# Kernel optimization log

Hardware: AMD Instinct MI355X
Metric: run time of the kernel (lower is better)

## Reference

```python
import math
import jax, jax.numpy as jnp
import numpy as np

B, N, NR, DA, E, H, NB = 2, 2048, 256, 256, 768, 12, 2
DH = E // H
NQ, NK = 32, 128
INF = 1e10


def _layernorm(x, g=None, b=None, eps=1e-5):
    mu = x.mean(-1, keepdims=True)
    var = ((x - mu) ** 2).mean(-1, keepdims=True)
    y = (x - mu) * jax.lax.rsqrt(var + eps)
    if g is not None:
        y = y * g + b
    return y


def _fourier(x):
    # NeRF-style: freqs = 2**linspace(0,12,64); out dim = 3*(1+2*64) = 387
    freqs = 2.0 ** jnp.linspace(0.0, 12.0, 64)
    ang = (x[..., None, :] * freqs[:, None]).reshape(*x.shape[:-1], -1)  # (...,192)
    return jnp.concatenate([x, jnp.sin(ang), jnp.cos(ang)], -1)


def _abs_pos(pos):
    # sinusoidal absolute PE, embed_dim=DA//2, include_input -> DA//2 + 1 dims
    d = DA // 2
    div = jnp.exp(jnp.arange(0, d, 2, dtype=jnp.float32) * (-math.log(10000.0) / d))
    ang = pos * div  # (B,N,1)*(d/2,) -> (B,N,d/2)
    return jnp.concatenate([pos, jnp.sin(ang), jnp.cos(ang)], -1)


def _local_bias(n, nq, nk):
    # vectorized create_local_attn_bias: block-diagonal local window mask
    i = jnp.arange(n)
    blk = i // nq
    lo = jnp.maximum(0, nq * blk - (nk - nq) // 2)
    hi = nq * blk + (nq + nk) // 2
    j = jnp.arange(n)
    allowed = (j[None, :] >= lo[:, None]) & (j[None, :] < hi[:, None])
    return jnp.where(allowed, 0.0, -INF).astype(jnp.float32)


def _rope(x, pos):
    # x: (B,H,N,DH), pos: (B,N) float
    half = DH // 2
    inv = 1.0 / (10000.0 ** (jnp.arange(half, dtype=jnp.float32) / half))
    ang = pos[:, None, :, None] * inv  # (B,1,N,half)
    c, s = jnp.cos(ang), jnp.sin(ang)
    x1, x2 = x[..., :half], x[..., half:]
    return jnp.concatenate([x1 * c - x2 * s, x1 * s + x2 * c], -1)


def setup_inputs() -> dict:
    key = jax.random.key(0)
    def rn(i, shape, s=1.0):
        return jax.random.normal(jax.random.fold_in(key, i), shape, jnp.float32) * s
    LF = 387 + (DA // 2 + 1) + 408  # 924
    tok = (jnp.arange(N) * NR) // N  # each atom's residue index (sorted)
    inp = {
        'atom_coords': rn(0, (B, N, 3), 10.0),
        'ref_pos': rn(1, (B, N, 3), 10.0),
        'res_id': jnp.broadcast_to(tok[None, :, None], (B, N, 1)).astype(jnp.int32),
        'res_type_feat': rn(2, (B, N, 23)),
        'charge': rn(3, (B, N, 1)),
        'atomic_number': rn(4, (B, N, 128)),
        'atom_name_feat': rn(5, (B, N, 256)),
        'adaLN_emb': rn(6, (B, DA)),
        'rope_pos': jnp.broadcast_to(jnp.arange(N, dtype=jnp.int32)[None], (B, N)),
        'atom_to_token': jnp.broadcast_to(jax.nn.one_hot(tok, NR, dtype=jnp.float32)[None], (B, N, NR)),
        'feat_W': rn(7, (LF, DA), 0.02), 'feat_b': jnp.zeros(DA), 'feat_ln_g': jnp.ones(DA), 'feat_ln_b': jnp.zeros(DA),
        'pos_W': rn(8, (387, DA), 0.02),
        'in_W': rn(9, (2 * DA, DA), 0.02),
        'tin_W': rn(10, (DA, E), 0.02), 'tin_b': jnp.zeros(E), 'tin_ln_g': jnp.ones(E), 'tin_ln_b': jnp.zeros(E),
        'ada_W': rn(11, (DA, E), 0.02), 'ada_b': jnp.zeros(E), 'ada_ln_g': jnp.ones(E), 'ada_ln_b': jnp.zeros(E),
        'blk_mod_W': rn(12, (NB, E, 6 * E), 0.02), 'blk_mod_b': jnp.zeros((NB, 6 * E)),
        'blk_qkv_W': rn(13, (NB, E, 3 * E), 0.02), 'blk_qkv_b': jnp.zeros((NB, 3 * E)),
        'blk_o_W': rn(14, (NB, E, E), 0.02), 'blk_o_b': jnp.zeros((NB, E)),
        'blk_m1_W': rn(15, (NB, E, 4 * E), 0.02), 'blk_m1_b': jnp.zeros((NB, 4 * E)),
        'blk_m2_W': rn(16, (NB, 4 * E, E), 0.02), 'blk_m2_b': jnp.zeros((NB, E)),
        'tout_W': rn(17, (E, DA), 0.02), 'tout_b': jnp.zeros(DA), 'tout_ln_g': jnp.ones(DA), 'tout_ln_b': jnp.zeros(DA),
    }
    return inp


def reference(atom_coords, ref_pos, res_id, res_type_feat, charge, atomic_number,
              atom_name_feat, adaLN_emb, rope_pos, atom_to_token,
              feat_W, feat_b, feat_ln_g, feat_ln_b, pos_W, in_W,
              tin_W, tin_b, tin_ln_g, tin_ln_b, ada_W, ada_b, ada_ln_g, ada_ln_b,
              blk_mod_W, blk_mod_b, blk_qkv_W, blk_qkv_b, blk_o_W, blk_o_b,
              blk_m1_W, blk_m1_b, blk_m2_W, blk_m2_b,
              tout_W, tout_b, tout_ln_g, tout_ln_b):
    # feature fusion
    ref_pos_emb = _fourier(ref_pos)                                   # (B,N,387)
    atom_res_pos = _abs_pos(res_id.astype(jnp.float32))               # (B,N,129)
    feats = jnp.concatenate([ref_pos_emb, res_type_feat, atom_res_pos,
                             charge, atomic_number, atom_name_feat], -1)  # (B,N,924)
    feats = jax.nn.silu(_layernorm(feats @ feat_W + feat_b, feat_ln_g, feat_ln_b))
    coords = _fourier(atom_coords) @ pos_W                            # (B,N,DA)
    atom_in = jnp.concatenate([feats, coords], -1) @ in_W             # (B,N,DA)
    x = _layernorm(atom_in @ tin_W + tin_b, tin_ln_g, tin_ln_b)       # (B,N,E)
    c = _layernorm(adaLN_emb @ ada_W + ada_b, ada_ln_g, ada_ln_b)     # (B,E)

    bias = _local_bias(N, NQ, NK)                                     # (N,N)
    pos = rope_pos.astype(jnp.float32)
    scale = 1.0 / math.sqrt(DH)
    for l in range(NB):  # small fixed layer count
        m = jax.nn.silu(c) @ blk_mod_W[l] + blk_mod_b[l]
        sh1, sc1, g1, sh2, sc2, g2 = jnp.split(m, 6, -1)              # each (B,E)
        h = _layernorm(x) * (1 + sc1[:, None]) + sh1[:, None]
        qkv = (h @ blk_qkv_W[l] + blk_qkv_b[l]).reshape(B, N, 3, H, DH)
        q, k, v = [qkv[:, :, i].transpose(0, 2, 1, 3) for i in range(3)]  # (B,H,N,DH)
        q, k = _rope(q, pos), _rope(k, pos)
        scores = jnp.einsum('bhqd,bhkd->bhqk', q, k) * scale + bias
        attn = jax.nn.softmax(scores, -1)
        o = jnp.einsum('bhqk,bhkd->bhqd', attn, v).transpose(0, 2, 1, 3).reshape(B, N, E)
        x = x + g1[:, None] * (o @ blk_o_W[l] + blk_o_b[l])
        h2 = _layernorm(x) * (1 + sc2[:, None]) + sh2[:, None]
        x = x + g2[:, None] * (jax.nn.gelu(h2 @ blk_m1_W[l] + blk_m1_b[l]) @ blk_m2_W[l] + blk_m2_b[l])

    atom_latent = _layernorm(x @ tout_W + tout_b, tout_ln_g, tout_ln_b)   # (B,N,DA)
    a2t = atom_to_token / (atom_to_token.sum(1, keepdims=True) + 1e-6)    # segment-mean weights
    residue_latent = jnp.einsum('bnr,bnd->brd', a2t, atom_latent)         # (B,NR,DA)
    return residue_latent, atom_latent
```

## Files before the change

kernel.cpp:

```cpp
#include <hip/hip_runtime.h>
#include <hip/hip_bf16.h>
#include <math.h>

#define B_ 2
#define N_ 2048
#define NR_ 256
#define DA_ 256
#define E_ 768
#define H_ 12
#define DH_ 64
#define NB_ 2

typedef __attribute__((ext_vector_type(8))) __bf16 bf16x8;
typedef __attribute__((ext_vector_type(4))) float f32x4;

union U8 { bf16x8 v; __hip_bfloat16 e[8]; unsigned short u[8]; };
union U4 { __hip_bfloat16 e[4]; uint2 u2; };

__device__ __forceinline__ void gload16(const void* g, void* l) {
    __builtin_amdgcn_global_load_lds(
        (const __attribute__((address_space(1))) void*)g,
        (__attribute__((address_space(3))) void*)l, 16, 0, 0);
}

__global__ __launch_bounds__(128) void build_feats_kernel(
    const float* __restrict__ atom_coords, const float* __restrict__ ref_pos,
    const int* __restrict__ res_id, const float* __restrict__ res_type,
    const float* __restrict__ charge, const float* __restrict__ atomic_number,
    const float* __restrict__ atom_name, const int* __restrict__ rope_pos,
    __hip_bfloat16* __restrict__ feats, __hip_bfloat16* __restrict__ coordsF,
    float* __restrict__ ropeC, float* __restrict__ ropeS)
{
    int a = blockIdx.x;
    int tid = threadIdx.x;
    __hip_bfloat16* f  = feats   + (size_t)a * 1024;
    __hip_bfloat16* cf = coordsF + (size_t)a * 512;

    float rp[3], cc[3];
    #pragma unroll
    for (int i = 0; i < 3; ++i) { rp[i] = ref_pos[(size_t)a*3 + i]; cc[i] = atom_coords[(size_t)a*3 + i]; }

    if (tid < 3) { f[tid] = __float2bfloat16(rp[tid]); cf[tid] = __float2bfloat16(cc[tid]); }

    if (tid >= 64 && tid < 96) {
        int dd = tid - 64;
        float rpos = (float)rope_pos[a];
        float ang = rpos * expf(-0.28782313662425574f * (float)dd);
        float sn, cs; sincosf(ang, &sn, &cs);
        ropeC[a*32 + dd] = cs; ropeS[a*32 + dd] = sn;
    }

    for (int s = tid; s < 192; s += 128) {
        int fi = s / 3, ci = s % 3;
        float freq = exp2f(12.f * (float)fi / 63.f);
        float ar = rp[ci] * freq;
        float ac = cc[ci] * freq;
        float snr, csr, snc, csc_;
        sincosf(ar, &snr, &csr);
        sincosf(ac, &snc, &csc_);
        f[3 + s]    = __float2bfloat16(snr);  f[195 + s]  = __float2bfloat16(csr);
        cf[3 + s]   = __float2bfloat16(snc);  cf[195 + s] = __float2bfloat16(csc_);
    }
    if (tid < 23) f[387 + tid] = __float2bfloat16(res_type[(size_t)a*23 + tid]);

    float pos = (float)res_id[a];
    if (tid == 0) f[410] = __float2bfloat16(pos);
    if (tid < 64) {
        float div = expf(-9.210340371976184f / 128.f * (float)(2 * tid));
        float ang = pos * div;
        float sn, cs; sincosf(ang, &sn, &cs);
        f[411 + tid] = __float2bfloat16(sn);
        f[475 + tid] = __float2bfloat16(cs);
    }
    if (tid == 0) f[539] = __float2bfloat16(charge[a]);
    if (tid < 128) f[540 + tid] = __float2bfloat16(atomic_number[(size_t)a*128 + tid]);
    for (int s = tid; s < 256; s += 128) f[668 + s] = __float2bfloat16(atom_name[(size_t)a*256 + s]);
    if (tid < 100) f[924 + tid] = __float2bfloat16(0.f);
    if (tid < 125) cf[387 + tid] = __float2bfloat16(0.f);
}

__global__ __launch_bounds__(256) void transconv_kernel(
    const float* __restrict__ W, __hip_bfloat16* __restrict__ WT,
    int Ksrc, int Kdst, int Nn, size_t wstride, size_t tstride)
{
    __shared__ float t[32][33];
    W  += (size_t)blockIdx.z * wstride;
    WT += (size_t)blockIdx.z * tstride;
    int n0 = blockIdx.x * 32, k0 = blockIdx.y * 32;
    int tid = threadIdx.x;
    int tx = tid & 31, ty = tid >> 5;
    #pragma unroll
    for (int i = 0; i < 4; ++i) {
        int k = k0 + ty + i*8;
        t[ty + i*8][tx] = (k < Ksrc) ? W[(size_t)k * Nn + n0 + tx] : 0.f;
    }
    __syncthreads();
    #pragma unroll
    for (int i = 0; i < 4; ++i) {
        int row = ty + i*8;
        WT[(size_t)(n0 + row) * Kdst + k0 + tx] = __float2bfloat16(t[tx][row]);
    }
}

__device__ __forceinline__ float epi_apply(float v, int grow, int gcol,
    const float* bias, int mode, const float* X, int ldx,
    const float* gate, int gstride)
{
    if (bias) v += bias[gcol];
    if (mode == 1) {
        float u = 1.5957691216057308f * (v + 0.044715f * v * v * v);
        v = v / (1.f + __expf(-u));
    } else if (mode == 2) {
        int b = grow >> 11;
        v = X[(size_t)grow * ldx + gcol] + gate[(size_t)b * gstride + gcol] * v;
    } else if (mode == 3) {
        v = v * gate[grow];
    }
    return v;
}

__global__ __launch_bounds__(256) void gemm_bf16_kernel(
    const __hip_bfloat16* __restrict__ A, int lda,
    const __hip_bfloat16* __restrict__ BT, int ldb,
    const float* __restrict__ bias,
    void* __restrict__ C, int ldc,
    int K, int mode, int obf,
    const float* __restrict__ X, int ldx,
    const float* __restrict__ gate, int gstride,
    float* __restrict__ P,
    int mtiles, size_t bstrideA, size_t bstrideB)
{
    __shared__ __hip_bfloat16 As[3][128 * 32];
    __shared__ __hip_bfloat16 Bs[3][128 * 32];

    int gx = gridDim.x;
    int nwg = gx * gridDim.y;
    int fo = blockIdx.y * gx + blockIdx.x;
    int ft = (fo & 7) * (nwg >> 3) + (fo >> 3);
    int bx = ft % gx, by = ft / gx;

    int bb  = by / mtiles;
    int m0l = (by % mtiles) * 128;
    int m0g = by * 128;
    int n0 = bx * 128;
    const __hip_bfloat16* Ab  = A  + (size_t)bb * bstrideA;
    const __hip_bfloat16* BTb = BT + (size_t)bb * bstrideB;
    int nz = gridDim.z;
    int Kh = K / nz;
    int kb = blockIdx.z * Kh;
    int nIter = Kh >> 5;
    int tid = threadIdx.x;
    int w = tid >> 6, l = tid & 63;
    int wr = (w >> 1) * 64, wc = (w & 1) * 64;
    int lr = l & 15, lg = l >> 4;
    int slot = ((lg ^ ((lr >> 1) & 3)) & 3) * 8;

    int seg0 = tid,        row0s = seg0 >> 2, g0 = (seg0 & 3) ^ ((row0s >> 1) & 3);
    int seg1 = 256 + tid,  row1s = seg1 >> 2, g1 = (seg1 & 3) ^ ((row1s >> 1) & 3);

    f32x4 acc[4][4];
    #pragma unroll
    for (int i = 0; i < 4; ++i)
        #pragma unroll
        for (int j = 0; j < 4; ++j)
            acc[i][j] = f32x4{0.f, 0.f, 0.f, 0.f};

    {
        gload16(Ab  + (size_t)(m0l + row0s) * lda + kb + g0 * 8, (char*)As[0] + seg0 * 16);
        gload16(BTb + (size_t)(n0 + row0s) * ldb + kb + g0 * 8, (char*)Bs[0] + seg0 * 16);
        gload16(Ab  + (size_t)(m0l + row1s) * lda + kb + g1 * 8, (char*)As[0] + seg1 * 16);
        gload16(BTb + (size_t)(n0 + row1s) * ldb + kb + g1 * 8, (char*)Bs[0] + seg1 * 16);
        if (nIter > 1) {
            int k1 = kb + 32;
            gload16(Ab  + (size_t)(m0l + row0s) * lda + k1 + g0 * 8, (char*)As[1] + seg0 * 16);
            gload16(BTb + (size_t)(n0 + row0s) * ldb + k1 + g0 * 8, (char*)Bs[1] + seg0 * 16);
            gload16(Ab  + (size_t)(m0l + row1s) * lda + k1 + g1 * 8, (char*)As[1] + seg1 * 16);
            gload16(BTb + (size_t)(n0 + row1s) * ldb + k1 + g1 * 8, (char*)Bs[1] + seg1 * 16);
        }
    }

    int cur = 0;
    for (int it = 0; it < nIter; ++it) {
        if (it + 1 < nIter) asm volatile("s_waitcnt vmcnt(4)" ::: "memory");
        else                asm volatile("s_waitcnt vmcnt(0)" ::: "memory");
        __builtin_amdgcn_s_barrier();
        __builtin_amdgcn_sched_barrier(0);
        if (it + 2 < nIter) {
            int nb = cur + 2; if (nb >= 3) nb -= 3;
            int kn = kb + (it + 2) * 32;
            gload16(Ab  + (size_t)(m0l + row0s) * lda + kn + g0 * 8, (char*)As[nb] + seg0 * 16);
            gload16(BTb + (size_t)(n0 + row0s) * ldb + kn + g0 * 8, (char*)Bs[nb] + seg0 * 16);
            gload16(Ab  + (size_t)(m0l + row1s) * lda + kn + g1 * 8, (char*)As[nb] + seg1 * 16);
            gload16(BTb + (size_t)(n0 + row1s) * ldb + kn + g1 * 8, (char*)Bs[nb] + seg1 * 16);
        }
        bf16x8 af[4], bfr[4];
        #pragma unroll
        for (int i = 0; i < 4; ++i) {
            af[i]  = *(bf16x8*)(As[cur] + (wr + i*16 + lr) * 32 + slot);
            bfr[i] = *(bf16x8*)(Bs[cur] + (wc + i*16 + lr) * 32 + slot);
        }
        #pragma unroll
        for (int i = 0; i < 4; ++i)
            #pragma unroll
            for (int j = 0; j < 4; ++j)
                acc[i][j] = __builtin_amdgcn_mfma_f32_16x16x32_bf16(af[i], bfr[j], acc[i][j], 0, 0, 0);
        cur = (cur == 2) ? 0 : cur + 1;
    }

    if (nz > 1) {
        int Nw = gridDim.x * 128;
        size_t pstride = (size_t)Nw * (gridDim.y * 128);
        float* Pz = P + (size_t)blockIdx.z * pstride;
        #pragma unroll
        for (int i = 0; i < 4; ++i)
            #pragma unroll
            for (int j = 0; j < 4; ++j)
                #pragma unroll
                for (int r = 0; r < 4; ++r) {
                    int grow = m0g + wr + i*16 + lg*4 + r;
                    int gcol = n0 + wc + j*16 + lr;
                    Pz[(size_t)grow * Nw + gcol] = acc[i][j][r];
                }
        return;
    }

    #pragma unroll
    for (int i = 0; i < 4; ++i)
        #pragma unroll
        for (int j = 0; j < 4; ++j)
            #pragma unroll
            for (int r = 0; r < 4; ++r) {
                int grow = m0g + wr + i*16 + lg*4 + r;
                int gcol = n0 + wc + j*16 + lr;
                float v = epi_apply(acc[i][j][r], grow, gcol, bias, mode, X, ldx, gate, gstride);
                if (obf)
                    ((__hip_bfloat16*)C)[(size_t)grow * ldc + gcol] = __float2bfloat16(v);
                else
                    ((float*)C)[(size_t)grow * ldc + gcol] = v;
            }
}

__global__ __launch_bounds__(256) void gcomb_kernel(
    const float* __restrict__ P, size_t pstride, int nz, int Nw,
    const float* __restrict__ bias,
    void* __restrict__ C, int ldc, int mode, int obf,
    const float* __restrict__ X, int ldx,
    const float* __restrict__ gate, int gstride,
    __hip_bfloat16* __restrict__ C2, int ldc2)
{
    int idx = blockIdx.x * 256 + threadIdx.x;
    int e0 = idx * 4;
    int grow = e0 / Nw, gc0 = e0 % Nw;
    float4 v = *(const float4*)(P + (size_t)grow * Nw + gc0);
    for (int z = 1; z < nz; ++z) {
        float4 t = *(const float4*)(P + (size_t)z * pstride + (size_t)grow * Nw + gc0);
        v.x += t.x; v.y += t.y; v.z += t.z; v.w += t.w;
    }
    float e[4] = {v.x, v.y, v.z, v.w};
    #pragma unroll
    for (int r = 0; r < 4; ++r)
        e[r] = epi_apply(e[r], grow, gc0 + r, bias, mode, X, ldx, gate, gstride);
    if (obf) {
        U4 o4;
        #pragma unroll
        for (int r = 0; r < 4; ++r) o4.e[r] = __float2bfloat16(e[r]);
        *(uint2*)((__hip_bfloat16*)C + (size_t)grow * ldc + gc0) = o4.u2;
    } else {
        *(float4*)((float*)C + (size_t)grow * ldc + gc0) = make_float4(e[0], e[1], e[2], e[3]);
    }
    if (C2) {
        U4 o4;
        #pragma unroll
        for (int r = 0; r < 4; ++r) o4.e[r] = __float2bfloat16(e[r]);
        *(uint2*)(C2 + (size_t)grow * ldc2 + gc0) = o4.u2;
    }
}

__global__ __launch_bounds__(256) void combln256_kernel(
    const float* __restrict__ P, size_t pstride, int nz,
    const float* __restrict__ bias,
    const float* __restrict__ g, const float* __restrict__ bv,
    int do_silu, int obf,
    void* __restrict__ out, int ldout)
{
    int row = blockIdx.x, d = threadIdx.x;
    __shared__ float red[256];
    float v = P[(size_t)row*256 + d];
    for (int z = 1; z < nz; ++z) v += P[(size_t)z*pstride + (size_t)row*256 + d];
    v += bias[d];
    red[d] = v; __syncthreads();
    for (int off = 128; off > 0; off >>= 1) { if (d < off) red[d] += red[d+off]; __syncthreads(); }
    float mu = red[0] * (1.f/256.f);
    __syncthreads();
    float dv = v - mu;
    red[d] = dv*dv; __syncthreads();
    for (int off = 128; off > 0; off >>= 1) { if (d < off) red[d] += red[d+off]; __syncthreads(); }
    float rstd = rsqrtf(red[0] * (1.f/256.f) + 1e-5f);
    float y = dv * rstd * g[d] + bv[d];
    if (do_silu) y = y / (1.f + __expf(-y));
    if (obf) ((__hip_bfloat16*)out)[(size_t)row * ldout + d] = __float2bfloat16(y);
    else     ((float*)out)[(size_t)row * ldout + d] = y;
}

__global__ __launch_bounds__(256) void gcombln_kernel(
    const float* __restrict__ P, size_t pstride, int nz,
    const float* __restrict__ bias,
    float* __restrict__ X,
    const float* __restrict__ gate,
    const float* __restrict__ scm, const float* __restrict__ shm,
    __hip_bfloat16* __restrict__ Hb)
{
    int row = blockIdx.x, tid = threadIdx.x;
    int b = row >> 11;
    __shared__ float red[256];
    float xv[3];
    float s = 0.f;
    #pragma unroll
    for (int q = 0; q < 3; ++q) {
        int d = tid + q*256;
        float v = P[(size_t)row*768 + d];
        for (int z = 1; z < nz; ++z) v += P[(size_t)z*pstride + (size_t)row*768 + d];
        v += bias[d];
        v = X[(size_t)row*768 + d] + gate[(size_t)b*4608 + d] * v;
        X[(size_t)row*768 + d] = v;
        xv[q] = v; s += v;
    }
    red[tid] = s; __syncthreads();
    for (int off = 128; off > 0; off >>= 1) { if (tid < off) red[tid] += red[tid+off]; __syncthreads(); }
    float mu = red[0] * (1.f/768.f);
    __syncthreads();
    float s2 = 0.f;
    #pragma unroll
    for (int q = 0; q < 3; ++q) { float dv = xv[q] - mu; s2 += dv*dv; }
    red[tid] = s2; __syncthreads();
    for (int off = 128; off > 0; off >>= 1) { if (tid < off) red[tid] += red[tid+off]; __syncthreads(); }
    float rstd = rsqrtf(red[0] * (1.f/768.f) + 1e-5f);
    #pragma unroll
    for (int q = 0; q < 3; ++q) {
        int d = tid + q*256;
        float y = (xv[q] - mu) * rstd * (1.f + scm[(size_t)b*4608 + d]) + shm[(size_t)b*4608 + d];
        Hb[(size_t)row*768 + d] = __float2bfloat16(y);
    }
}

__global__ __launch_bounds__(256) void rownorm_kernel(
    const float* __restrict__ in, int ldin,
    void* __restrict__ out, int ldout,
    int D, int mode, int obf,
    const float* __restrict__ gvec, const float* __restrict__ bvec,
    const float* __restrict__ scm, const float* __restrict__ shm, int mstride)
{
    int row = blockIdx.x;
    int tid = threadIdx.x;
    __shared__ float red[256];
    const float* pin = in + (size_t)row * ldin;
    float vals[3];
    float s = 0.f;
    #pragma unroll
    for (int q = 0; q < 3; ++q) {
        int d = tid + q*256;
        float v = (d < D) ? pin[d] : 0.f;
        vals[q] = v; s += v;
    }
    red[tid] = s; __syncthreads();
    for (int off = 128; off > 0; off >>= 1) { if (tid < off) red[tid] += red[tid+off]; __syncthreads(); }
    float mu = red[0] / (float)D;
    __syncthreads();
    float s2 = 0.f;
    #pragma unroll
    for (int q = 0; q < 3; ++q) { int d = tid + q*256; if (d < D) { float dv = vals[q] - mu; s2 += dv*dv; } }
    red[tid] = s2; __syncthreads();
    for (int off = 128; off > 0; off >>= 1) { if (tid < off) red[tid] += red[tid+off]; __syncthreads(); }
    float rstd = rsqrtf(red[0] / (float)D + 1e-5f);
    int b = row / N_;
    #pragma unroll
    for (int q = 0; q < 3; ++q) {
        int d = tid + q*256;
        if (d >= D) continue;
        float y = (vals[q] - mu) * rstd;
        if (mode & 1) y = y * gvec[d] + bvec[d];
        if (mode & 2) y = y * (1.f + scm[(size_t)b*mstride + d]) + shm[(size_t)b*mstride + d];
        if (mode & 4) y = y / (1.f + expf(-y));
        if (obf) ((__hip_bfloat16*)out)[(size_t)row * ldout + d] = __float2bfloat16(y);
        else     ((float*)out)[(size_t)row * ldout + d] = y;
    }
}

__global__ __launch_bounds__(256) void ada_kernel(
    const float* __restrict__ emb, const float* __restrict__ W,
    const float* __restrict__ bias,
    const float* __restrict__ g, const float* __restrict__ bb,
    float* __restrict__ c, float* __restrict__ c_silu)
{
    int b = blockIdx.x, tid = threadIdx.x;
    __shared__ float emb_s[256];
    __shared__ float t[768];
    __shared__ float red[256];
    emb_s[tid] = emb[b*256 + tid];
    __syncthreads();
    for (int q = 0; q < 3; ++q) {
        int e = tid + q*256;
        float acc = bias[e];
        for (int k = 0; k < 256; ++k) acc += emb_s[k] * W[(size_t)k*768 + e];
        t[e] = acc;
    }
    __syncthreads();
    float s = 0.f; for (int q = 0; q < 3; ++q) s += t[tid + q*256];
    red[tid] = s; __syncthreads();
    for (int off = 128; off > 0; off >>= 1) { if (tid < off) red[tid] += red[tid+off]; __syncthreads(); }
    float mu = red[0] / 768.f; __syncthreads();
    float s2 = 0.f; for (int q = 0; q < 3; ++q) { float d = t[tid + q*256] - mu; s2 += d*d; }
    red[tid] = s2; __syncthreads();
    for (int off = 128; off > 0; off >>= 1) { if (tid < off) red[tid] += red[tid+off]; __syncthreads(); }
    float rstd = rsqrtf(red[0] / 768.f + 1e-5f);
    for (int q = 0; q < 3; ++q) {
        int e = tid + q*256;
        float y = (t[e] - mu) * rstd * g[e] + bb[e];
        c[b*768 + e] = y;
        c_silu[b*768 + e] = y / (1.f + expf(-y));
    }
}

__global__ __launch_bounds__(256) void mod2_kernel(
    const float* __restrict__ c_silu, const float* __restrict__ mod_W,
    float* __restrict__ part)
{
    int idx = blockIdx.x * 256 + threadIdx.x;
    int z = blockIdx.y;
    int lyr = idx / 9216, b = (idx / 4608) & 1, j = idx % 4608;
    const float* Wl = mod_W + (size_t)lyr * 768 * 4608;
    const float* cs = c_silu + b * 768;
    float acc = 0.f;
    int k0 = z * 192;
    for (int k = k0; k < k0 + 192; ++k) acc += cs[k] * Wl[(size_t)k * 4608 + j];
    part[(size_t)z * 18432 + idx] = acc;
}

__global__ __launch_bounds__(256) void modc_kernel(
    const float* __restrict__ part, const float* __restrict__ mod_b,
    float* __restrict__ m2buf)
{
    int idx = blockIdx.x * 256 + threadIdx.x;
    int lyr = idx / 9216, j = idx % 4608;
    float acc = mod_b[(size_t)lyr * 4608 + j];
    #pragma unroll
    for (int z = 0; z < 4; ++z) acc += part[(size_t)z * 18432 + idx];
    m2buf[idx] = acc;
}

__global__ __launch_bounds__(64) void attn_mfma_kernel(
    const __hip_bfloat16* __restrict__ qkv,
    const float* __restrict__ ropeC,
    const float* __restrict__ ropeS,
    __hip_bfloat16* __restrict__ o)
{
    int bid = blockIdx.x;
    int qb = bid & 63;
    int h  = (bid >> 6) % 12;
    int b  = bid / 768;
    int l  = threadIdx.x;
    int lr = l & 15, lg = l >> 4;
    int lo = max(0, 32*qb - 48);
    int hi = min(N_, 32*qb + 80);
    int wlen = hi - lo;

    __shared__ __hip_bfloat16 Vl[128 * 72];
    __shared__ __hip_bfloat16 Pl[32 * 144];

    {
        int vr0 = l >> 3;
        int c0  = (l & 7) * 8;
        #pragma unroll
        for (int it = 0; it < 16; ++it) {
            int vr = it*8 + vr0;
            int n = lo + vr;
            U8 v;
            if (n < hi) {
                v.v = *(const bf16x8*)(qkv + ((size_t)(b*N_ + n))*2304 + 1536 + h*64 + c0);
            } else {
                #pragma unroll
                for (int j = 0; j < 8; ++j) v.u[j] = 0;
            }
            *(bf16x8*)(Vl + vr*72 + c0) = v.v;
        }
    }

    bf16x8 aq0[2], aq1[2];
    #pragma unroll
    for (int i = 0; i < 2; ++i) {
        int n = qb*32 + i*16 + lr;
        const __hip_bfloat16* qrow = qkv + ((size_t)(b*N_ + n))*2304 + h*64;
        U8 xlo, xhi;
        xlo.v = *(const bf16x8*)(qrow + lg*8);
        xhi.v = *(const bf16x8*)(qrow + 32 + lg*8);
        const float* pc = ropeC + ((size_t)(b*N_ + n))*32 + lg*8;
        const float* ps = ropeS + ((size_t)(b*N_ + n))*32 + lg*8;
        float4 c0 = *(const float4*)(pc), c1 = *(const float4*)(pc + 4);
        float4 s0 = *(const float4*)(ps), s1 = *(const float4*)(ps + 4);
        float cv[8] = {c0.x,c0.y,c0.z,c0.w,c1.x,c1.y,c1.z,c1.w};
        float sv[8] = {s0.x,s0.y,s0.z,s0.w,s1.x,s1.y,s1.z,s1.w};
        U8 f0, f1;
        #pragma unroll
        for (int j = 0; j < 8; ++j) {
            float x1 = __bfloat162float(xlo.e[j]);
            float x2 = __bfloat162float(xhi.e[j]);
            f0.e[j] = __float2bfloat16(x1*cv[j] - x2*sv[j]);
            f1.e[j] = __float2bfloat16(x1*sv[j] + x2*cv[j]);
        }
        aq0[i] = f0.v; aq1[i] = f1.v;
    }

    f32x4 S[2][8];
    #pragma unroll
    for (int i = 0; i < 2; ++i)
        #pragma unroll
        for (int jt = 0; jt < 8; ++jt)
            S[i][jt] = f32x4{0.f, 0.f, 0.f, 0.f};

    #pragma unroll
    for (int jt = 0; jt < 8; ++jt) {
        int n = lo + jt*16 + lr;
        U8 f0, f1;
        if (n < hi) {
            const __hip_bfloat16* krow = qkv + ((size_t)(b*N_ + n))*2304 + 768 + h*64;
            U8 xlo, xhi;
            xlo.v = *(const bf16x8*)(krow + lg*8);
            xhi.v = *(const bf16x8*)(krow + 32 + lg*8);
            const float* pc = ropeC + ((size_t)(b*N_ + n))*32 + lg*8;
            const float* ps = ropeS + ((size_t)(b*N_ + n))*32 + lg*8;
            float4 c0 = *(const float4*)(pc), c1 = *(const float4*)(pc + 4);
            float4 s0 = *(const float4*)(ps), s1 = *(const float4*)(ps + 4);
            float cv[8] = {c0.x,c0.y,c0.z,c0.w,c1.x,c1.y,c1.z,c1.w};
            float sv[8] = {s0.x,s0.y,s0.z,s0.w,s1.x,s1.y,s1.z,s1.w};
            #pragma unroll
            for (int j = 0; j < 8; ++j) {
                float x1 = __bfloat162float(xlo.e[j]);
                float x2 = __bfloat162float(xhi.e[j]);
                f0.e[j] = __float2bfloat16(x1*cv[j] - x2*sv[j]);
                f1.e[j] = __float2bfloat16(x1*sv[j] + x2*cv[j]);
            }
        } else {
            #pragma unroll
            for (int j = 0; j < 8; ++j) { f0.u[j] = 0; f1.u[j] = 0; }
        }
        #pragma unroll
        for (int i = 0; i < 2; ++i) {
            S[i][jt] = __builtin_amdgcn_mfma_f32_16x16x32_bf16(aq0[i], f0.v, S[i][jt], 0, 0, 0);
            S[i][jt] = __builtin_amdgcn_mfma_f32_16x16x32_bf16(aq1[i], f1.v, S[i][jt], 0, 0, 0);
        }
    }

    #pragma unroll
    for (int jt = 0; jt < 8; ++jt) {
        bool oob = (jt*16 + lr) >= wlen;
        #pragma unroll
        for (int i = 0; i < 2; ++i)
            #pragma unroll
            for (int r = 0; r < 4; ++r)
                S[i][jt][r] = oob ? -1e30f : S[i][jt][r] * 0.125f;
    }

    float rinv[2][4];
    #pragma unroll
    for (int i = 0; i < 2; ++i) {
        #pragma unroll
        for (int r = 0; r < 4; ++r) {
            float m = -1e30f;
            #pragma unroll
            for (int jt = 0; jt < 8; ++jt) m = fmaxf(m, S[i][jt][r]);
            #pragma unroll
            for (int mask = 8; mask > 0; mask >>= 1) m = fmaxf(m, __shfl_xor(m, mask, 16));
            float sum = 0.f;
            #pragma unroll
            for (int jt = 0; jt < 8; ++jt) {
                float e = __expf(S[i][jt][r] - m);
                S[i][jt][r] = e;
                sum += e;
            }
            #pragma unroll
            for (int mask = 8; mask > 0; mask >>= 1) sum += __shfl_xor(sum, mask, 16);
            rinv[i][r] = 1.f / sum;
        }
    }

    #pragma unroll
    for (int i = 0; i < 2; ++i)
        #pragma unroll
        for (int jt = 0; jt < 8; ++jt)
            #pragma unroll
            for (int r = 0; r < 4; ++r) {
                int row = i*16 + lg*4 + r;
                int colp = (jt*16 + lr) ^ (lg << 3);
                Pl[row*144 + colp] = __float2bfloat16(S[i][jt][r]);
            }

    __syncthreads();

    f32x4 O_[2][4];
    #pragma unroll
    for (int i = 0; i < 2; ++i)
        #pragma unroll
        for (int ct = 0; ct < 4; ++ct)
            O_[i][ct] = f32x4{0.f, 0.f, 0.f, 0.f};

    int key = (lr >> 2) & 3;
    #pragma unroll
    for (int kt = 0; kt < 4; ++kt) {
        bf16x8 pa[2];
        #pragma unroll
        for (int i = 0; i < 2; ++i) {
            int row = i*16 + lr;
            int colp = (kt*32 + lg*8) ^ (key << 3);
            pa[i] = *(bf16x8*)(Pl + row*144 + colp);
        }
        #pragma unroll
        for (int ct = 0; ct < 4; ++ct) {
            U8 bv;
            #pragma unroll
            for (int j = 0; j < 8; ++j)
                bv.e[j] = Vl[(kt*32 + lg*8 + j)*72 + ct*16 + lr];
            O_[0][ct] = __builtin_amdgcn_mfma_f32_16x16x32_bf16(pa[0], bv.v, O_[0][ct], 0, 0, 0);
            O_[1][ct] = __builtin_amdgcn_mfma_f32_16x16x32_bf16(pa[1], bv.v, O_[1][ct], 0, 0, 0);
        }
    }

    #pragma unroll
    for (int i = 0; i < 2; ++i)
        #pragma unroll
        for (int ct = 0; ct < 4; ++ct)
            #pragma unroll
            for (int r = 0; r < 4; ++r) {
                int row = qb*32 + i*16 + lg*4 + r;
                o[((size_t)(b*N_ + row))*768 + h*64 + ct*16 + lr] =
                    __float2bfloat16(O_[i][ct][r] * rinv[i][r]);
            }
}

__global__ __launch_bounds__(256) void a2t_transpose_kernel(
    const float* __restrict__ a2t, __hip_bfloat16* __restrict__ a2tTb)
{
    __shared__ float t[32][33];
    int r0 = blockIdx.x * 32, n0 = blockIdx.y * 32, b = blockIdx.z;
    int tid = threadIdx.x;
    int tx = tid & 31, ty = tid >> 5;
    #pragma unroll
    for (int i = 0; i < 4; ++i) {
        int row = ty + i*8;
        t[row][tx] = a2t[((size_t)b*N_ + n0 + row) * 256 + r0 + tx];
    }
    __syncthreads();
    #pragma unroll
    for (int i = 0; i < 4; ++i) {
        int row = ty + i*8;
        a2tTb[((size_t)b*256 + r0 + row) * N_ + n0 + tx] = __float2bfloat16(t[tx][row]);
    }
}

__global__ __launch_bounds__(256) void rowrecip_kernel(
    const __hip_bfloat16* __restrict__ a2tTb, float* __restrict__ recip)
{
    int row = blockIdx.x;
    int tid = threadIdx.x;
    __shared__ float red[256];
    U8 v; v.v = *(const bf16x8*)(a2tTb + (size_t)row*2048 + tid*8);
    float s = 0.f;
    #pragma unroll
    for (int j = 0; j < 8; ++j) s += __bfloat162float(v.e[j]);
    red[tid] = s; __syncthreads();
    for (int off = 128; off > 0; off >>= 1) { if (tid < off) red[tid] += red[tid+off]; __syncthreads(); }
    if (tid == 0) recip[row] = 1.f / (red[0] + 1e-6f);
}

extern "C" void kernel_launch(void* const* d_in, const int* in_sizes, int n_in,
                              void* d_out, int out_size, void* d_ws, size_t ws_size,
                              hipStream_t stream) {
    const float* atom_coords  = (const float*)d_in[0];
    const float* ref_pos      = (const float*)d_in[1];
    const int*   res_id       = (const int*)  d_in[2];
    const float* res_type     = (const float*)d_in[3];
    const float* charge       = (const float*)d_in[4];
    const float* atomic_num   = (const float*)d_in[5];
    const float* atom_name    = (const float*)d_in[6];
    const float* adaLN_emb    = (const float*)d_in[7];
    const int*   rope_pos     = (const int*)  d_in[8];
    const float* atom_to_tok  = (const float*)d_in[9];
    const float* feat_W       = (const float*)d_in[10];
    const float* feat_b       = (const float*)d_in[11];
    const float* feat_ln_g    = (const float*)d_in[12];
    const float* feat_ln_b    = (const float*)d_in[13];
    const float* pos_W        = (const float*)d_in[14];
    const float* in_W         = (const float*)d_in[15];
    const float* tin_W        = (const float*)d_in[16];
    const float* tin_b        = (const float*)d_in[17];
    const float* tin_ln_g     = (const float*)d_in[18];
    const float* tin_ln_b     = (const float*)d_in[19];
    const float* ada_W        = (const float*)d_in[20];
    const float* ada_b        = (const float*)d_in[21];
    const float* ada_ln_g     = (const float*)d_in[22];
    const float* ada_ln_b     = (const float*)d_in[23];
    const float* blk_mod_W    = (const float*)d_in[24];
    const float* blk_mod_b    = (const float*)d_in[25];
    const float* blk_qkv_W    = (const float*)d_in[26];
    const float* blk_qkv_b    = (const float*)d_in[27];
    const float* blk_o_W      = (const float*)d_in[28];
    const float* blk_o_b      = (const float*)d_in[29];
    const float* blk_m1_W     = (const float*)d_in[30];
    const float* blk_m1_b     = (const float*)d_in[31];
    const float* blk_m2_W     = (const float*)d_in[32];
    const float* blk_m2_b     = (const float*)d_in[33];
    const float* tout_W       = (const float*)d_in[34];
    const float* tout_b       = (const float*)d_in[35];
    const float* tout_ln_g    = (const float*)d_in[36];
    const float* tout_ln_b    = (const float*)d_in[37];

    const int BN = B_ * N_;
    float* ws = (float*)d_ws;

    const size_t OFF_X    = 0;
    const size_t OFF_HB   = OFF_X    + (size_t)BN*768;
    const size_t OFF_QKVB = OFF_HB   + (size_t)BN*768/2;
    const size_t OFF_OB   = OFF_QKVB + (size_t)BN*2304/2;
    const size_t OFF_UB   = OFF_OB   + (size_t)BN*768/2;
    const size_t OFF_WT   = OFF_UB   + (size_t)BN*3072/2;
    const size_t OFF_RC   = OFF_WT   + (size_t)3072*768/2;
    const size_t OFF_RS   = OFF_RC   + (size_t)BN*32;
    const size_t OFF_SM   = OFF_RS   + (size_t)BN*32;

    float* X = ws + OFF_X;
    __hip_bfloat16* Hb   = (__hip_bfloat16*)(ws + OFF_HB);
    __hip_bfloat16* QKVb = (__hip_bfloat16*)(ws + OFF_QKVB);
    __hip_bfloat16* Ob   = (__hip_bfloat16*)(ws + OFF_OB);
    __hip_bfloat16* Ub   = (__hip_bfloat16*)(ws + OFF_UB);
    __hip_bfloat16* WT   = (__hip_bfloat16*)(ws + OFF_WT);
    float* ropeC  = ws + OFF_RC;
    float* ropeS  = ws + OFF_RS;
    float* cbuf   = ws + OFF_SM;
    float* c_silu = cbuf + 1536;
    float* mbuf2  = c_silu + 1536;
    float* modpart= mbuf2 + 18432;

    __hip_bfloat16* featsB  = QKVb;
    __hip_bfloat16* coordsB = QKVb + (size_t)BN*1024;
    float* t1               = ws + OFF_UB;
    __hip_bfloat16* concatB = (__hip_bfloat16*)(t1 + (size_t)BN*256);
    __hip_bfloat16* atom_inB= Ob;

    __hip_bfloat16* a2tTb   = Ob;
    __hip_bfloat16* latTb   = Ob + (size_t)2*256*2048;
    float* recip            = modpart;

    float* P_pa   = ws + OFF_X;
    float* P_tin  = ws + OFF_UB;
    float* P_o    = ws + OFF_UB;
    float* P_m2   = ws + OFF_QKVB;
    float* P_tout = ws + OFF_UB;
    float* P_res  = ws + OFF_UB;

    float* out_res = (float*)d_out;
    float* out_lat = out_res + (size_t)B_*NR_*DA_;

    build_feats_kernel<<<BN, 128, 0, stream>>>(atom_coords, ref_pos, res_id,
        res_type, charge, atomic_num, atom_name, rope_pos, featsB, coordsB,
        ropeC, ropeS);

    transconv_kernel<<<dim3(8, 32), 256, 0, stream>>>(feat_W, WT, 924, 1024, 256, 0, 0);
    gemm_bf16_kernel<<<dim3(2, 32, 4), 256, 0, stream>>>(featsB, 1024, WT, 1024, nullptr,
        nullptr, 0, 1024, 0, 0, nullptr, 0, nullptr, 0, P_pa, 32, 0, 0);
    combln256_kernel<<<BN, 256, 0, stream>>>(P_pa, (size_t)BN*256, 4, feat_b,
        feat_ln_g, feat_ln_b, 1, 1, concatB, 512);
    transconv_kernel<<<dim3(8, 16), 256, 0, stream>>>(pos_W, WT, 387, 512, 256, 0, 0);
    gemm_bf16_kernel<<<dim3(2, 32, 4), 256, 0, stream>>>(coordsB, 512, WT, 512, nullptr,
        nullptr, 0, 512, 0, 0, nullptr, 0, nullptr, 0, P_pa, 32, 0, 0);
    gcomb_kernel<<<1024, 256, 0, stream>>>(P_pa, (size_t)BN*256, 4, 256, nullptr,
        concatB + 256, 512, 0, 1, nullptr, 0, nullptr, 0, nullptr, 0);
    transconv_kernel<<<dim3(8, 16), 256, 0, stream>>>(in_W, WT, 512, 512, 256, 0, 0);
    gemm_bf16_kernel<<<dim3(2, 32, 4), 256, 0, stream>>>(concatB, 512, WT, 512, nullptr,
        nullptr, 0, 512, 0, 0, nullptr, 0, nullptr, 0, P_pa, 32, 0, 0);
    gcomb_kernel<<<1024, 256, 0, stream>>>(P_pa, (size_t)BN*256, 4, 256, nullptr,
        atom_inB, 256, 0, 1, nullptr, 0, nullptr, 0, nullptr, 0);
    transconv_kernel<<<dim3(24, 8), 256, 0, stream>>>(tin_W, WT, 256, 256, 768, 0, 0);
    gemm_bf16_kernel<<<dim3(6, 32, 2), 256, 0, stream>>>(atom_inB, 256, WT, 256, nullptr,
        nullptr, 0, 256, 0, 0, nullptr, 0, nullptr, 0, P_tin, 32, 0, 0);
    gcomb_kernel<<<3072, 256, 0, stream>>>(P_tin, (size_t)BN*768, 2, 768, tin_b,
        X, 768, 0, 0, nullptr, 0, nullptr, 0, nullptr, 0);
    rownorm_kernel<<<BN, 256, 0, stream>>>(X, 768, X, 768, 768, 1, 0,
        tin_ln_g, tin_ln_b, nullptr, nullptr, 0);

    ada_kernel<<<2, 256, 0, stream>>>(adaLN_emb, ada_W, ada_b, ada_ln_g, ada_ln_b,
        cbuf, c_silu);
    mod2_kernel<<<dim3(72, 4), 256, 0, stream>>>(c_silu, blk_mod_W, modpart);
    modc_kernel<<<72, 256, 0, stream>>>(modpart, blk_mod_b, mbuf2);

    for (int l = 0; l < NB_; ++l) {
        const float* qkvW = blk_qkv_W + (size_t)l*768*2304;
        const float* qkvB = blk_qkv_b + (size_t)l*2304;
        const float* oW   = blk_o_W   + (size_t)l*768*768;
        const float* oB   = blk_o_b   + (size_t)l*768;
        const float* m1W  = blk_m1_W  + (size_t)l*768*3072;
        const float* m1B  = blk_m1_b  + (size_t)l*3072;
        const float* m2W  = blk_m2_W  + (size_t)l*3072*768;
        const float* m2B  = blk_m2_b  + (size_t)l*768;

        float* mptr = mbuf2 + (size_t)l*9216;
        float* sh1 = mptr + 0,    *sc1 = mptr + 768,  *g1 = mptr + 1536;
        float* sh2 = mptr + 2304, *sc2 = mptr + 3072, *g2 = mptr + 3840;

        if (l == 0)
            rownorm_kernel<<<BN, 256, 0, stream>>>(X, 768, Hb, 768, 768, 2, 1,
                nullptr, nullptr, sc1, sh1, 4608);
        transconv_kernel<<<dim3(72, 24), 256, 0, stream>>>(qkvW, WT, 768, 768, 2304, 0, 0);
        gemm_bf16_kernel<<<dim3(18, 32, 1), 256, 0, stream>>>(Hb, 768, WT, 768, qkvB,
            QKVb, 2304, 768, 0, 1, nullptr, 0, nullptr, 0, nullptr, 32, 0, 0);
        attn_mfma_kernel<<<B_*H_*64, 64, 0, stream>>>(QKVb, ropeC, ropeS, Ob);
        transconv_kernel<<<dim3(24, 24), 256, 0, stream>>>(oW, WT, 768, 768, 768, 0, 0);
        gemm_bf16_kernel<<<dim3(6, 32, 2), 256, 0, stream>>>(Ob, 768, WT, 768, nullptr,
            nullptr, 0, 768, 0, 0, nullptr, 0, nullptr, 0, P_o, 32, 0, 0);
        gcombln_kernel<<<BN, 256, 0, stream>>>(P_o, (size_t)BN*768, 2, oB,
            X, g1, sc2, sh2, Hb);
        transconv_kernel<<<dim3(96, 24), 256, 0, stream>>>(m1W, WT, 768, 768, 3072, 0, 0);
        gemm_bf16_kernel<<<dim3(24, 32, 1), 256, 0, stream>>>(Hb, 768, WT, 768, m1B,
            Ub, 3072, 768, 1, 1, nullptr, 0, nullptr, 0, nullptr, 32, 0, 0);
        transconv_kernel<<<dim3(24, 96), 256, 0, stream>>>(m2W, WT, 3072, 3072, 768, 0, 0);
        gemm_bf16_kernel<<<dim3(6, 32, 2), 256, 0, stream>>>(Ub, 3072, WT, 3072, nullptr,
            nullptr, 0, 3072, 0, 0, nullptr, 0, nullptr, 0, P_m2, 32, 0, 0);
        if (l < NB_ - 1) {
            float* mnext = mbuf2 + (size_t)(l+1)*9216;
            gcombln_kernel<<<BN, 256, 0, stream>>>(P_m2, (size_t)BN*768, 2, m2B,
                X, g2, mnext + 768, mnext + 0, Hb);
        } else {
            gcomb_kernel<<<3072, 256, 0, stream>>>(P_m2, (size_t)BN*768, 2, 768, m2B,
                X, 768, 2, 0, X, 768, g2, 4608, Hb, 768);
        }
    }

    transconv_kernel<<<dim3(8, 24), 256, 0, stream>>>(tout_W, WT, 768, 768, 256, 0, 0);
    gemm_bf16_kernel<<<dim3(2, 32, 4), 256, 0, stream>>>(Hb, 768, WT, 768, nullptr,
        nullptr, 0, 768, 0, 0, nullptr, 0, nullptr, 0, P_tout, 32, 0, 0);
    combln256_kernel<<<BN, 256, 0, stream>>>(P_tout, (size_t)BN*256, 4, tout_b,
        tout_ln_g, tout_ln_b, 0, 0, out_lat, 256);

    a2t_transpose_kernel<<<dim3(8, 64, 2), 256, 0, stream>>>(atom_to_tok, a2tTb);
    rowrecip_kernel<<<512, 256, 0, stream>>>(a2tTb, recip);
    transconv_kernel<<<dim3(8, 64, 2), 256, 0, stream>>>(out_lat, latTb, 2048, 2048, 256,
        (size_t)2048*256, (size_t)256*2048);
    gemm_bf16_kernel<<<dim3(2, 4, 8), 256, 0, stream>>>(a2tTb, 2048, latTb, 2048, nullptr,
        nullptr, 0, 2048, 0, 0, nullptr, 0, nullptr, 0, P_res,
        2, (size_t)256*2048, (size_t)256*2048);
    gcomb_kernel<<<128, 256, 0, stream>>>(P_res, (size_t)512*256, 8, 256, nullptr,
        out_res, 256, 3, 0, nullptr, 0, recip, 0, nullptr, 0);
}
```

Baseline: 613.0 us.

## Add LDS-free register-direct bf16 GEMM and drop split-K for out-projection

Adds a GEMM variant that loads A and B fragments straight from global memory into registers, with register double-buffering, instead of staging through a triple-buffered LDS pipeline. The QKV, out-projection, MLP1 and MLP2 GEMMs in the transformer blocks now use it. The out-projection no longer splits K and writes fp32 output directly to P_o, so the combine kernel reads one partial instead of two. The aim is to remove LDS traffic and synchronisation overhead. In exchange, operand data shared across waves is no longer reused from LDS, loads are strided row reads, and the out-projection runs with half as many workgroups.

```diff
diff --git a/kernel.cpp b/kernel.cpp
--- a/kernel.cpp
+++ b/kernel.cpp
@@ -117,6 +117,108 @@
         v = v * gate[grow];
     }
     return v;
+}
+
+__global__ __launch_bounds__(256) void gemm_bf16_direct_kernel(
+    const __hip_bfloat16* __restrict__ A, int lda,
+    const __hip_bfloat16* __restrict__ BT, int ldb,
+    const float* __restrict__ bias,
+    void* __restrict__ C, int ldc,
+    int K, int mode, int obf,
+    const float* __restrict__ X, int ldx,
+    const float* __restrict__ gate, int gstride,
+    float* __restrict__ P)
+{
+    int gx = gridDim.x;
+    int nwg = gx * gridDim.y;
+    int fo = blockIdx.y * gx + blockIdx.x;
+    int ft = (fo & 7) * (nwg >> 3) + (fo >> 3);
+    int bx = ft % gx, by = ft / gx;
+
+    int m0 = by * 128, n0 = bx * 128;
+    int nz = gridDim.z;
+    int Kh = K / nz;
+    int kb = blockIdx.z * Kh;
+    int nIter = Kh >> 5;
+    int tid = threadIdx.x;
+    int w = tid >> 6, l = tid & 63;
+    int wr = (w >> 1) * 64, wc = (w & 1) * 64;
+    int lr = l & 15, lg = l >> 4;
+
+    const __hip_bfloat16* pA[4];
+    const __hip_bfloat16* pB[4];
+    #pragma unroll
+    for (int i = 0; i < 4; ++i) {
+        pA[i] = A  + (size_t)(m0 + wr + i*16 + lr) * lda + kb + lg*8;
+        pB[i] = BT + (size_t)(n0 + wc + i*16 + lr) * ldb + kb + lg*8;
+    }
+
+    f32x4 acc[4][4];
+    #pragma unroll
+    for (int i = 0; i < 4; ++i)
+        #pragma unroll
+        for (int j = 0; j < 4; ++j)
+            acc[i][j] = f32x4{0.f, 0.f, 0.f, 0.f};
+
+    bf16x8 a0[4], b0[4], a1[4], b1[4];
+    #pragma unroll
+    for (int i = 0; i < 4; ++i) { a0[i] = *(const bf16x8*)(pA[i]); b0[i] = *(const bf16x8*)(pB[i]); }
+
+    for (int it = 0; it < nIter; it += 2) {
+        int k1 = (it + 1) * 32, k2 = (it + 2) * 32;
+        if (it + 1 < nIter) {
+            #pragma unroll
+            for (int i = 0; i < 4; ++i) { a1[i] = *(const bf16x8*)(pA[i] + k1); b1[i] = *(const bf16x8*)(pB[i] + k1); }
+        }
+        #pragma unroll
+        for (int i = 0; i < 4; ++i)
+            #pragma unroll
+            for (int j = 0; j < 4; ++j)
+                acc[i][j] = __builtin_amdgcn_mfma_f32_16x16x32_bf16(a0[i], b0[j], acc[i][j], 0, 0, 0);
+        if (it + 2 < nIter) {
+            #pragma unroll
+            for (int i = 0; i < 4; ++i) { a0[i] = *(const bf16x8*)(pA[i] + k2); b0[i] = *(const bf16x8*)(pB[i] + k2); }
+        }
+        if (it + 1 < nIter) {
+            #pragma unroll
+            for (int i = 0; i < 4; ++i)
+                #pragma unroll
+                for (int j = 0; j < 4; ++j)
+                    acc[i][j] = __builtin_amdgcn_mfma_f32_16x16x32_bf16(a1[i], b1[j], acc[i][j], 0, 0, 0);
+        }
+    }
+
+    if (nz > 1) {
+        int Nw = gridDim.x * 128;
+        size_t pstride = (size_t)Nw * (gridDim.y * 128);
+        float* Pz = P + (size_t)blockIdx.z * pstride;
+        #pragma unroll
+        for (int i = 0; i < 4; ++i)
+            #pragma unroll
+            for (int j = 0; j < 4; ++j)
+                #pragma unroll
+                for (int r = 0; r < 4; ++r) {
+                    int grow = m0 + wr + i*16 + lg*4 + r;
+                    int gcol = n0 + wc + j*16 + lr;
+                    Pz[(size_t)grow * Nw + gcol] = acc[i][j][r];
+                }
+        return;
+    }
+
+    #pragma unroll
+    for (int i = 0; i < 4; ++i)
+        #pragma unroll
+        for (int j = 0; j < 4; ++j)
+            #pragma unroll
+            for (int r = 0; r < 4; ++r) {
+                int grow = m0 + wr + i*16 + lg*4 + r;
+                int gcol = n0 + wc + j*16 + lr;
+                float v = epi_apply(acc[i][j][r], grow, gcol, bias, mode, X, ldx, gate, gstride);
+                if (obf)
+                    ((__hip_bfloat16*)C)[(size_t)grow * ldc + gcol] = __float2bfloat16(v);
+                else
+                    ((float*)C)[(size_t)grow * ldc + gcol] = v;
+            }
 }
 
 __global__ __launch_bounds__(256) void gemm_bf16_kernel(
@@ -809,20 +911,20 @@
             rownorm_kernel<<<BN, 256, 0, stream>>>(X, 768, Hb, 768, 768, 2, 1,
                 nullptr, nullptr, sc1, sh1, 4608);
         transconv_kernel<<<dim3(72, 24), 256, 0, stream>>>(qkvW, WT, 768, 768, 2304, 0, 0);
-        gemm_bf16_kernel<<<dim3(18, 32, 1), 256, 0, stream>>>(Hb, 768, WT, 768, qkvB,
-            QKVb, 2304, 768, 0, 1, nullptr, 0, nullptr, 0, nullptr, 32, 0, 0);
+        gemm_bf16_direct_kernel<<<dim3(18, 32, 1), 256, 0, stream>>>(Hb, 768, WT, 768, qkvB,
+            QKVb, 2304, 768, 0, 1, nullptr, 0, nullptr, 0, nullptr);
         attn_mfma_kernel<<<B_*H_*64, 64, 0, stream>>>(QKVb, ropeC, ropeS, Ob);
         transconv_kernel<<<dim3(24, 24), 256, 0, stream>>>(oW, WT, 768, 768, 768, 0, 0);
-        gemm_bf16_kernel<<<dim3(6, 32, 2), 256, 0, stream>>>(Ob, 768, WT, 768, nullptr,
-            nullptr, 0, 768, 0, 0, nullptr, 0, nullptr, 0, P_o, 32, 0, 0);
-        gcombln_kernel<<<BN, 256, 0, stream>>>(P_o, (size_t)BN*768, 2, oB,
+        gemm_bf16_direct_kernel<<<dim3(6, 32, 1), 256, 0, stream>>>(Ob, 768, WT, 768, nullptr,
+            P_o, 768, 768, 0, 0, nullptr, 0, nullptr, 0, nullptr);
+        gcombln_kernel<<<BN, 256, 0, stream>>>(P_o, (size_t)BN*768, 1, oB,
             X, g1, sc2, sh2, Hb);
         transconv_kernel<<<dim3(96, 24), 256, 0, stream>>>(m1W, WT, 768, 768, 3072, 0, 0);
-        gemm_bf16_kernel<<<dim3(24, 32, 1), 256, 0, stream>>>(Hb, 768, WT, 768, m1B,
-            Ub, 3072, 768, 1, 1, nullptr, 0, nullptr, 0, nullptr, 32, 0, 0);
+        gemm_bf16_direct_kernel<<<dim3(24, 32, 1), 256, 0, stream>>>(Hb, 768, WT, 768, m1B,
+            Ub, 3072, 768, 1, 1, nullptr, 0, nullptr, 0, nullptr);
         transconv_kernel<<<dim3(24, 96), 256, 0, stream>>>(m2W, WT, 3072, 3072, 768, 0, 0);
-        gemm_bf16_kernel<<<dim3(6, 32, 2), 256, 0, stream>>>(Ub, 3072, WT, 3072, nullptr,
-            nullptr, 0, 3072, 0, 0, nullptr, 0, nullptr, 0, P_m2, 32, 0, 0);
+        gemm_bf16_direct_kernel<<<dim3(6, 32, 2), 256, 0, stream>>>(Ub, 3072, WT, 3072, nullptr,
+            nullptr, 0, 3072, 0, 0, nullptr, 0, nullptr, 0, P_m2);
         if (l < NB_ - 1) {
             float* mnext = mbuf2 + (size_t)(l+1)*9216;
             gcombln_kernel<<<BN, 256, 0, stream>>>(P_m2, (size_t)BN*768, 2, m2B,
```

Result: slower. 956.0 us (+56.0%).
